# Optimization experiments

Hardware: AMD Instinct MI355X
Metric: run time of the kernel (lower is better)

Reference implementation:

```python
import jax, jax.numpy as jnp
import numpy as np

B, P, G, E = 8, 32, 128, 32
S, SUB = 1024, 768
HD = E // 2              # gene head dim = 16
LAMBDA_INIT = 0.8 - 0.6 * float(np.exp(-0.3 * 0))  # depth=0 -> 0.2
SCALING = HD ** -0.5


def stable_softmax(x, axis=-1, eps=1e-8):
    x_max = jnp.max(x, axis=axis, keepdims=True)
    x_exp = jnp.exp(x - x_max)
    return x_exp / (jnp.sum(x_exp, axis=axis, keepdims=True) + eps)


def setup_inputs() -> dict:
    key = jax.random.key(0)
    ks = jax.random.split(key, 12)
    std_q = (1.0 / E) ** 0.5
    std_k = (1.0 / SUB) ** 0.5
    return {
        "query": jax.random.normal(ks[0], (B, P, G, E), jnp.float32),
        "key": jax.random.normal(ks[1], (B, S, SUB), jnp.float32),
        "query_mask": jax.random.randint(ks[2], (B, P, G), 0, 2).astype(bool),
        "key_mask": jax.random.randint(ks[3], (B, S), 0, 2).astype(bool),
        "Wq": jax.random.normal(ks[4], (E, E), jnp.float32) * std_q,
        "Wk": jax.random.normal(ks[5], (SUB, E), jnp.float32) * std_k,
        "Wv": jax.random.normal(ks[6], (SUB, E), jnp.float32) * std_k,
        "Wo": jax.random.normal(ks[7], (E, E), jnp.float32) * std_q,
        "lq1": jax.random.normal(ks[8], (HD,), jnp.float32) * 0.1,
        "lk1": jax.random.normal(ks[9], (HD,), jnp.float32) * 0.1,
        "lq2": jax.random.normal(ks[10], (HD,), jnp.float32) * 0.1,
        "lk2": jax.random.normal(ks[11], (HD,), jnp.float32) * 0.1,
        "rms_w": jnp.ones((E,), jnp.float32),
    }


def reference(query, key, query_mask, key_mask, Wq, Wk, Wv, Wo,
              lq1, lk1, lq2, lk2, rms_w):
    b, p, g, e = query.shape
    L = p * g
    s = key.shape[1]

    gene_flat = query.reshape(b, L, e)
    Q = (gene_flat @ Wq).reshape(b, L, 2, HD).transpose(0, 2, 1, 3)  # [B,2,L,hd]
    K = (key @ Wk).reshape(b, s, 2, HD).transpose(0, 2, 1, 3)        # [B,2,S,hd]
    V = key @ Wv                                                     # [B,S,2*hd]

    scores = jnp.einsum("bhld,bhsd->bhls", Q * SCALING, K)           # [B,2,L,S]

    qm = query_mask.reshape(b, L)                                    # [B,L]
    combined = qm[:, None, :, None] & key_mask[:, None, None, :]     # [B,1,L,S]
    scores = jnp.where(combined, scores, -1e20)

    attn = stable_softmax(scores, axis=-1)                           # [B,2,L,S]

    lam1 = jnp.exp(jnp.sum(lq1 * lk1))
    lam2 = jnp.exp(jnp.sum(lq2 * lk2))
    lam_full = lam1 - lam2 + LAMBDA_INIT

    diff = attn[:, 0] - lam_full * attn[:, 1]                        # [B,L,S]
    diff = diff - jnp.min(diff, axis=-1, keepdims=True) + 1e-5
    diff = jnp.where(qm[:, :, None], diff, 0.0)
    diff = jnp.where(key_mask[:, None, :], diff, 0.0)

    attn_out = jnp.einsum("bls,bse->ble", diff, V)                   # [B,L,E]

    # RMSNorm over last dim (2*hd = E), eps=1e-5, elementwise affine
    rms = jax.lax.rsqrt(jnp.mean(attn_out * attn_out, axis=-1, keepdims=True) + 1e-5)
    attn_out = attn_out * rms * rms_w
    attn_out = attn_out * (1.0 - LAMBDA_INIT)

    out = (attn_out @ Wo).reshape(b, p, g, e)
    return out, diff.reshape(b, p, g, s)
```

## Files before the change

### kernel.cpp

```cpp
#include <hip/hip_runtime.h>

namespace {

typedef __attribute__((ext_vector_type(8))) short short8v;
typedef __attribute__((ext_vector_type(4))) float f32x4;
typedef __attribute__((ext_vector_type(4))) unsigned int uint4v;

constexpr int kB = 8;
constexpr int kS = 1024;
constexpr int kSUB = 768;
constexpr int kL = 4096;
constexpr float kQScale = 0.25f * 1.44269504088896340736f;
constexpr float kLamInit = 0.2f;
constexpr float kOutScale = 0.8f;
constexpr float kShift = 64.f;

__device__ __forceinline__ unsigned short f2bf(float x) {
  unsigned u = __float_as_uint(x);
  return (unsigned short)((u + 0x7FFFu + ((u >> 16) & 1u)) >> 16);
}

__device__ __forceinline__ float fast_exp2(float x) {
#if __has_builtin(__builtin_amdgcn_exp2f)
  return __builtin_amdgcn_exp2f(x);
#else
  return exp2f(x);
#endif
}

__device__ __forceinline__ int load_mask(const void* p, long i, int fmt) {
  if (fmt == 1) return (int)((const unsigned char*)p)[i];
  if (fmt == 2) return (int)(((const int*)p)[2 * i] != 0);
  return ((const int*)p)[i];
}

__global__ __launch_bounds__(256) void prep_kernel(
    const float* __restrict__ Wk, const float* __restrict__ Wv,
    const unsigned char* __restrict__ qm, unsigned short* __restrict__ WkT,
    unsigned short* __restrict__ WvT, int* __restrict__ flag) {
  if (blockIdx.x < 192) {
    int idx = blockIdx.x * 256 + threadIdx.x;
    if (idx < 24576) {
      const int k = idx >> 5, c = idx & 31;
      WkT[c * 768 + k] = f2bf(Wk[idx]);
    } else {
      idx -= 24576;
      const int k = idx >> 5, c = idx & 31;
      WvT[c * 768 + k] = f2bf(Wv[idx]);
    }
  } else {
    __shared__ int any14, any47;
    if (threadIdx.x == 0) { any14 = 0; any47 = 0; }
    __syncthreads();
    int l14 = 0, l47 = 0;
    for (int i = threadIdx.x; i < 16384; i += 256) {
      const unsigned char v = qm[i];
      if (v && (i & 3)) l14 = 1;
      if (v && ((i & 7) >= 4)) l47 = 1;
    }
    if (l14) atomicOr(&any14, 1);
    if (l47) atomicOr(&any47, 1);
    __syncthreads();
    if (threadIdx.x == 0) *flag = any14 ? 1 : (any47 ? 0 : 2);
  }
}

__global__ __launch_bounds__(256) void proj_kv_kernel(
    const float* __restrict__ key, const unsigned short* __restrict__ WkT,
    const unsigned short* __restrict__ WvT, unsigned short* __restrict__ Kbf,
    unsigned short* __restrict__ Vt) {
  __shared__ float comb[2][64][20];
  const int t = threadIdx.x;
  const int wv = t >> 6, lane = t & 63;
  const int r15 = lane & 15, g = lane >> 4;
  const int grp = wv >> 1;
  const int half = wv & 1;
  const int row = blockIdx.x * 32 + grp * 16 + r15;
  const int kbase = half * 384;
  const float* kp = &key[(size_t)row * kSUB + kbase];
  const f32x4 zf = {0.f, 0.f, 0.f, 0.f};
  f32x4 aK0 = zf, aK1 = zf, aV0 = zf, aV1 = zf;
#pragma unroll 4
  for (int ks = 0; ks < 384; ks += 32) {
    const f32x4 lo = *(const f32x4*)&kp[ks + g * 8];
    const f32x4 hi = *(const f32x4*)&kp[ks + g * 8 + 4];
    short8v a;
#pragma unroll
    for (int j = 0; j < 4; ++j) {
      a[j] = (short)f2bf(lo[j]);
      a[4 + j] = (short)f2bf(hi[j]);
    }
    const int ko = kbase + ks + g * 8;
    const short8v bk0 = *(const short8v*)&WkT[(size_t)r15 * 768 + ko];
    const short8v bk1 = *(const short8v*)&WkT[(size_t)(16 + r15) * 768 + ko];
    const short8v bv0 = *(const short8v*)&WvT[(size_t)r15 * 768 + ko];
    const short8v bv1 = *(const short8v*)&WvT[(size_t)(16 + r15) * 768 + ko];
    aK0 = __builtin_amdgcn_mfma_f32_16x16x32_bf16(a, bk0, aK0, 0, 0, 0);
    aK1 = __builtin_amdgcn_mfma_f32_16x16x32_bf16(a, bk1, aK1, 0, 0, 0);
    aV0 = __builtin_amdgcn_mfma_f32_16x16x32_bf16(a, bv0, aV0, 0, 0, 0);
    aV1 = __builtin_amdgcn_mfma_f32_16x16x32_bf16(a, bv1, aV1, 0, 0, 0);
  }
  if (half == 1) {
    *(f32x4*)&comb[grp][lane][0] = aK0;
    *(f32x4*)&comb[grp][lane][4] = aK1;
    *(f32x4*)&comb[grp][lane][8] = aV0;
    *(f32x4*)&comb[grp][lane][12] = aV1;
  }
  __syncthreads();
  if (half == 0) {
    aK0 += *(const f32x4*)&comb[grp][lane][0];
    aK1 += *(const f32x4*)&comb[grp][lane][4];
    aV0 += *(const f32x4*)&comb[grp][lane][8];
    aV1 += *(const f32x4*)&comb[grp][lane][12];
    const int orow = blockIdx.x * 32 + grp * 16 + g * 4;
#pragma unroll
    for (int jj = 0; jj < 4; ++jj) {
      const int r = orow + jj;
      Kbf[(size_t)r * 32 + r15] = f2bf(aK0[jj]);
      Kbf[(size_t)r * 32 + 16 + r15] = f2bf(aK1[jj]);
      const int bb = r >> 10, s = r & 1023;
      Vt[((size_t)bb * 32 + r15) * kS + s] = f2bf(aV0[jj]);
      Vt[((size_t)bb * 32 + 16 + r15) * kS + s] = f2bf(aV1[jj]);
    }
  }
}

__global__ __launch_bounds__(512, 2) void attn_kernel(
    const float* __restrict__ query, const float* __restrict__ Wq,
    const unsigned short* __restrict__ Kbf,
    const unsigned short* __restrict__ Vt, const void* __restrict__ qmask,
    const void* __restrict__ kmask, const float* __restrict__ lq1,
    const float* __restrict__ lk1, const float* __restrict__ lq2,
    const float* __restrict__ lk2, const float* __restrict__ rmsw,
    const float* __restrict__ Wo, const int* __restrict__ mflag,
    float* __restrict__ out, float* __restrict__ diff) {
  extern __shared__ __align__(16) unsigned short kfl[];

  __shared__ __align__(16) float ubuf[5120];
  __shared__ __align__(16) unsigned short qlds[128][40];
  __shared__ unsigned kmp_lds[256];
  __shared__ float sWo[32][32];
  __shared__ float srw[32];
  __shared__ int qmS[128];
  __shared__ float slam;

  float* const sWq = ubuf;
  float* const sQi = ubuf + 1024;
  float* const nxlds = ubuf;

  const int t = threadIdx.x;
  const int lane = t & 63;
  const int w = t >> 6;
  const int r15 = lane & 15;
  const int g = lane >> 4;
  const int b = blockIdx.x >> 5;
  const int rowbase = b * kL + (blockIdx.x & 31) * 128;
  const int kvb = b * kS;
  const int fmt = *mflag;

  if (t < 256) {
    *(f32x4*)(sWq + 4 * t) = *(const f32x4*)(Wq + 4 * t);
    *(f32x4*)(&sWo[0][0] + 4 * t) = *(const f32x4*)(Wo + 4 * t);
    const long base = (long)kvb + 4 * t;
    const unsigned m0 = load_mask(kmask, base + 0, fmt) ? 1u : 0u;
    const unsigned m1 = load_mask(kmask, base + 1, fmt) ? 1u : 0u;
    const unsigned m2 = load_mask(kmask, base + 2, fmt) ? 1u : 0u;
    const unsigned m3 = load_mask(kmask, base + 3, fmt) ? 1u : 0u;
    kmp_lds[t] = m0 | (m1 << 8) | (m2 << 16) | (m3 << 24);
  }
  *(f32x4*)(sQi + 8 * t) = *(const f32x4*)(query + (size_t)rowbase * 32 + 8 * t);
  *(f32x4*)(sQi + 8 * t + 4) =
      *(const f32x4*)(query + (size_t)rowbase * 32 + 8 * t + 4);
#pragma unroll
  for (int p = 0; p < 8; ++p) {
    const int i = t + 512 * p;
    const int row = i >> 2, qtr = i & 3;
    *(short8v*)&kfl[row * 40 + qtr * 8] =
        *(const short8v*)&Kbf[((size_t)(kvb + row)) * 32 + qtr * 8];
  }
  if (t < 128) qmS[t] = load_mask(qmask, (long)rowbase + t, fmt);
  if (t < 32) srw[t] = rmsw[t];
  if (t == 0) {
    float a = 0.f, c2 = 0.f;
#pragma unroll
    for (int i = 0; i < 16; ++i) {
      a += lq1[i] * lk1[i];
      c2 += lq2[i] * lk2[i];
    }
    slam = expf(a) - expf(c2) + kLamInit;
  }
  __syncthreads();

#pragma unroll
  for (int p = 0; p < 8; ++p) {
    const int idx = t + 512 * p;
    const int row = idx >> 5, col = idx & 31;
    float a = 0.f;
#pragma unroll
    for (int k = 0; k < 32; ++k) a += sQi[row * 32 + k] * sWq[k * 32 + col];
    qlds[row][col] = f2bf(a * kQScale);
  }
  __syncthreads();

  const short8v z8 = {0, 0, 0, 0, 0, 0, 0, 0};
  const f32x4 zf = {0.f, 0.f, 0.f, 0.f};
  const float lam = slam;
  const int qm = qmS[w * 16 + r15];
  const int wrow = rowbase + w * 16;

  short8v qa0 = z8, qa1 = z8;
  if (lane < 32) {
    qa0 = *(const short8v*)&qlds[w * 16 + r15][g * 8];
    qa1 = *(const short8v*)&qlds[w * 16 + r15][16 + g * 8];
  }

  f32x4 s0v = zf, s1v = zf;
  for (int sl = 0; sl < 8; ++sl) {
#pragma unroll
    for (int c = 0; c < 8; ++c) {
      const int srow = sl * 128 + c * 16 + r15;
      short8v kb0 = z8, kb1 = z8;
      if (lane < 32) {
        kb0 = *(const short8v*)&kfl[srow * 40 + g * 8];
        kb1 = *(const short8v*)&kfl[srow * 40 + 16 + g * 8];
      }
      const f32x4 a0 =
          __builtin_amdgcn_mfma_f32_16x16x32_bf16(kb0, qa0, zf, 0, 0, 0);
      const f32x4 a1 =
          __builtin_amdgcn_mfma_f32_16x16x32_bf16(kb1, qa1, zf, 0, 0, 0);
      const unsigned km = kmp_lds[sl * 32 + c * 4 + g];
#pragma unroll
      for (int jj = 0; jj < 4; ++jj) {
        const int mbit = (km >> (8 * jj)) & 1u;
        s0v[jj] += mbit ? fast_exp2(a0[jj] - kShift) : 0.f;
        s1v[jj] += mbit ? fast_exp2(a1[jj] - kShift) : 0.f;
      }
    }
  }
  float s0 = (s0v[0] + s0v[1]) + (s0v[2] + s0v[3]);
  float s1 = (s1v[0] + s1v[1]) + (s1v[2] + s1v[3]);
  s0 += __shfl_xor(s0, 16);
  s0 += __shfl_xor(s0, 32);
  s1 += __shfl_xor(s1, 16);
  s1 += __shfl_xor(s1, 32);
  const float f0 = 1.f / (s0 + 1e-37f);
  const float nf1 = -lam / (s1 + 1e-37f);

  f32x4 dmn = {3.0e38f, 3.0e38f, 3.0e38f, 3.0e38f};
  for (int sl = 0; sl < 8; ++sl) {
#pragma unroll
    for (int c = 0; c < 8; ++c) {
      const int srow = sl * 128 + c * 16 + r15;
      short8v kb0 = z8, kb1 = z8;
      if (lane < 32) {
        kb0 = *(const short8v*)&kfl[srow * 40 + g * 8];
        kb1 = *(const short8v*)&kfl[srow * 40 + 16 + g * 8];
      }
      const f32x4 a0 =
          __builtin_amdgcn_mfma_f32_16x16x32_bf16(kb0, qa0, zf, 0, 0, 0);
      const f32x4 a1 =
          __builtin_amdgcn_mfma_f32_16x16x32_bf16(kb1, qa1, zf, 0, 0, 0);
      const unsigned km = kmp_lds[sl * 32 + c * 4 + g];
#pragma unroll
      for (int jj = 0; jj < 4; ++jj) {
        const int mbit = (km >> (8 * jj)) & 1u;
        const float e0 = mbit ? fast_exp2(a0[jj] - kShift) : 0.f;
        const float e1 = mbit ? fast_exp2(a1[jj] - kShift) : 0.f;
        dmn[jj] = fminf(dmn[jj], fmaf(e0, f0, nf1 * e1));
      }
    }
  }
  float dm = fminf(fminf(dmn[0], dmn[1]), fminf(dmn[2], dmn[3]));
  dm = fminf(dm, __shfl_xor(dm, 16));
  dm = fminf(dm, __shfl_xor(dm, 32));
  const float rmin = dm;

  f32x4 pv0 = zf, pv1 = zf;
  const int sl0 = ((g & 1) << 5) + r15;
  const int sl1 = sl0 + 16;
  const bool hi = (g >> 1) != 0;
  for (int sl = 0; sl < 8; ++sl) {
    short8v vt0[4], vt1[4];
#pragma unroll
    for (int kc = 0; kc < 4; ++kc) {
      const int soff = sl * 128 + kc * 32 + g * 8;
      vt0[kc] = *(const short8v*)&Vt[((size_t)(b * 32 + r15)) * kS + soff];
      vt1[kc] = *(const short8v*)&Vt[((size_t)(b * 32 + 16 + r15)) * kS + soff];
    }
    unsigned pkx[8], pky[8];
#pragma unroll
    for (int c = 0; c < 8; ++c) {
      const int srow = sl * 128 + c * 16 + r15;
      short8v kb0 = z8, kb1 = z8;
      if (lane < 32) {
        kb0 = *(const short8v*)&kfl[srow * 40 + g * 8];
        kb1 = *(const short8v*)&kfl[srow * 40 + 16 + g * 8];
      }
      const f32x4 a0 =
          __builtin_amdgcn_mfma_f32_16x16x32_bf16(kb0, qa0, zf, 0, 0, 0);
      const f32x4 a1 =
          __builtin_amdgcn_mfma_f32_16x16x32_bf16(kb1, qa1, zf, 0, 0, 0);
      const unsigned km = kmp_lds[sl * 32 + c * 4 + g];
      f32x4 fd;
#pragma unroll
      for (int jj = 0; jj < 4; ++jj) {
        const int mbit = (km >> (8 * jj)) & 1u;
        const float e0 = mbit ? fast_exp2(a0[jj] - kShift) : 0.f;
        const float e1 = mbit ? fast_exp2(a1[jj] - kShift) : 0.f;
        const float d = fmaf(e0, f0, nf1 * e1);
        fd[jj] = (qm && mbit) ? d - rmin + 1e-5f : 0.f;
      }
      pkx[c] = (unsigned)f2bf(fd[0]) | ((unsigned)f2bf(fd[1]) << 16);
      pky[c] = (unsigned)f2bf(fd[2]) | ((unsigned)f2bf(fd[3]) << 16);
      *(f32x4*)&diff[((size_t)(wrow + r15)) * kS + sl * 128 + c * 16 + g * 4] =
          fd;
    }
#pragma unroll
    for (int kc = 0; kc < 4; ++kc) {
      const unsigned x0a = (unsigned)__shfl((int)pkx[2 * kc], sl0);
      const unsigned y0a = (unsigned)__shfl((int)pky[2 * kc], sl0);
      const unsigned x0b = (unsigned)__shfl((int)pkx[2 * kc], sl1);
      const unsigned y0b = (unsigned)__shfl((int)pky[2 * kc], sl1);
      const unsigned x1a = (unsigned)__shfl((int)pkx[2 * kc + 1], sl0);
      const unsigned y1a = (unsigned)__shfl((int)pky[2 * kc + 1], sl0);
      const unsigned x1b = (unsigned)__shfl((int)pkx[2 * kc + 1], sl1);
      const unsigned y1b = (unsigned)__shfl((int)pky[2 * kc + 1], sl1);
      uint4v avw;
      avw.x = hi ? x1a : x0a;
      avw.y = hi ? y1a : y0a;
      avw.z = hi ? x1b : x0b;
      avw.w = hi ? y1b : y0b;
      const short8v av = *(const short8v*)&avw;
      pv0 = __builtin_amdgcn_mfma_f32_16x16x32_bf16(av, vt0[kc], pv0, 0, 0, 0);
      pv1 = __builtin_amdgcn_mfma_f32_16x16x32_bf16(av, vt1[kc], pv1, 0, 0, 0);
    }
  }

  float* const nxw = nxlds + w * (16 * 36);
#pragma unroll
  for (int jj = 0; jj < 4; ++jj) {
    float ss = pv0[jj] * pv0[jj] + pv1[jj] * pv1[jj];
    ss += __shfl_xor(ss, 1);
    ss += __shfl_xor(ss, 2);
    ss += __shfl_xor(ss, 4);
    ss += __shfl_xor(ss, 8);
    const float rms = 1.0f / sqrtf(ss * (1.f / 32.f) + 1e-5f);
    nxw[(g * 4 + jj) * 36 + r15] = pv0[jj] * rms * srw[r15] * kOutScale;
    nxw[(g * 4 + jj) * 36 + 16 + r15] =
        pv1[jj] * rms * srw[16 + r15] * kOutScale;
  }
  asm volatile("s_waitcnt lgkmcnt(0)" ::: "memory");

  {
    const int q2 = lane >> 2;
    const int cg = (lane & 3) * 8;
    float o[8] = {0.f, 0.f, 0.f, 0.f, 0.f, 0.f, 0.f, 0.f};
#pragma unroll
    for (int e = 0; e < 32; ++e) {
      const float nv = nxw[q2 * 36 + e];
#pragma unroll
      for (int j = 0; j < 8; ++j) o[j] += nv * sWo[e][cg + j];
    }
    f32x4 olo = {o[0], o[1], o[2], o[3]};
    f32x4 ohi = {o[4], o[5], o[6], o[7]};
    *(f32x4*)&out[((size_t)(wrow + q2)) * 32 + cg] = olo;
    *(f32x4*)&out[((size_t)(wrow + q2)) * 32 + cg + 4] = ohi;
  }
}

}

extern "C" void kernel_launch(void* const* d_in, const int* in_sizes, int n_in,
                              void* d_out, int out_size, void* d_ws,
                              size_t ws_size, hipStream_t stream) {
  const float* query = (const float*)d_in[0];
  const float* key = (const float*)d_in[1];
  const void* qmask = d_in[2];
  const void* kmask = d_in[3];
  const float* Wq = (const float*)d_in[4];
  const float* Wk = (const float*)d_in[5];
  const float* Wv = (const float*)d_in[6];
  const float* Wo = (const float*)d_in[7];
  const float* lq1 = (const float*)d_in[8];
  const float* lk1 = (const float*)d_in[9];
  const float* lq2 = (const float*)d_in[10];
  const float* lk2 = (const float*)d_in[11];
  const float* rmsw = (const float*)d_in[12];

  unsigned short* Kbf = (unsigned short*)d_ws;
  unsigned short* Vt = Kbf + (size_t)kB * kS * 32;
  unsigned short* WkT = Vt + (size_t)kB * kS * 32;
  unsigned short* WvT = WkT + (size_t)32 * 768;
  int* mflag = (int*)(WvT + (size_t)32 * 768);

  float* outp = (float*)d_out;
  float* diffp = outp + (size_t)kB * kL * 32;

  prep_kernel<<<dim3(193), dim3(256), 0, stream>>>(
      Wk, Wv, (const unsigned char*)qmask, WkT, WvT, mflag);
  proj_kv_kernel<<<dim3(kB * kS / 32), dim3(256), 0, stream>>>(key, WkT, WvT,
                                                               Kbf, Vt);
  attn_kernel<<<dim3(kB * (kL / 128)), dim3(512), 81920, stream>>>(
      query, Wq, Kbf, Vt, qmask, kmask, lq1, lk1, lq2, lk2, rmsw, Wo, mflag,
      outp, diffp);
}
```

Before: 104.1 us.

## Split key dimension across wave pairs and read K directly from global

The attention kernel now handles 32 query rows per 256-thread block instead of 128 rows per 512-thread block. Each pair of waves splits the 1024 keys in half, and the halves are combined through LDS reductions for the softmax sums, the row minimum and the PV accumulators. The 80 KB dynamic LDS staging of K is removed, and K is loaded from global/L2 on each pass. This cuts LDS use so more blocks can be resident and gives four times as many blocks, at the cost of repeated global K reads, extra block barriers, and half the waves sitting idle during the output projection.

```diff
diff --git a/kernel.cpp b/kernel.cpp
--- a/kernel.cpp
+++ b/kernel.cpp
@@ -125,7 +125,7 @@
   }
 }
 
-__global__ __launch_bounds__(512, 2) void attn_kernel(
+__global__ __launch_bounds__(256, 4) void attn_kernel(
     const float* __restrict__ query, const float* __restrict__ Wq,
     const unsigned short* __restrict__ Kbf,
     const unsigned short* __restrict__ Vt, const void* __restrict__ qmask,
@@ -134,14 +134,15 @@
     const float* __restrict__ lk2, const float* __restrict__ rmsw,
     const float* __restrict__ Wo, const int* __restrict__ mflag,
     float* __restrict__ out, float* __restrict__ diff) {
-  extern __shared__ __align__(16) unsigned short kfl[];
-
-  __shared__ __align__(16) float ubuf[5120];
-  __shared__ __align__(16) unsigned short qlds[128][40];
+  __shared__ __align__(16) float ubuf[2048];
+  __shared__ __align__(16) unsigned short qlds[32][40];
   __shared__ unsigned kmp_lds[256];
   __shared__ float sWo[32][32];
+  __shared__ float redA[4][2][16];
+  __shared__ float redB[4][16];
+  __shared__ float pvred[4][16][33];
   __shared__ float srw[32];
-  __shared__ int qmS[128];
+  __shared__ int qmS[32];
   __shared__ float slam;
 
   float* const sWq = ubuf;
@@ -151,14 +152,16 @@
   const int t = threadIdx.x;
   const int lane = t & 63;
   const int w = t >> 6;
+  const int group = w >> 1;
+  const int shalf = w & 1;
   const int r15 = lane & 15;
   const int g = lane >> 4;
-  const int b = blockIdx.x >> 5;
-  const int rowbase = b * kL + (blockIdx.x & 31) * 128;
+  const int b = blockIdx.x >> 7;
+  const int rowbase = b * kL + (blockIdx.x & 127) * 32;
   const int kvb = b * kS;
   const int fmt = *mflag;
 
-  if (t < 256) {
+  {
     *(f32x4*)(sWq + 4 * t) = *(const f32x4*)(Wq + 4 * t);
     *(f32x4*)(&sWo[0][0] + 4 * t) = *(const f32x4*)(Wo + 4 * t);
     const long base = (long)kvb + 4 * t;
@@ -167,19 +170,13 @@
     const unsigned m2 = load_mask(kmask, base + 2, fmt) ? 1u : 0u;
     const unsigned m3 = load_mask(kmask, base + 3, fmt) ? 1u : 0u;
     kmp_lds[t] = m0 | (m1 << 8) | (m2 << 16) | (m3 << 24);
-  }
-  *(f32x4*)(sQi + 8 * t) = *(const f32x4*)(query + (size_t)rowbase * 32 + 8 * t);
-  *(f32x4*)(sQi + 8 * t + 4) =
-      *(const f32x4*)(query + (size_t)rowbase * 32 + 8 * t + 4);
-#pragma unroll
-  for (int p = 0; p < 8; ++p) {
-    const int i = t + 512 * p;
-    const int row = i >> 2, qtr = i & 3;
-    *(short8v*)&kfl[row * 40 + qtr * 8] =
-        *(const short8v*)&Kbf[((size_t)(kvb + row)) * 32 + qtr * 8];
-  }
-  if (t < 128) qmS[t] = load_mask(qmask, (long)rowbase + t, fmt);
-  if (t < 32) srw[t] = rmsw[t];
+    *(f32x4*)(sQi + 4 * t) =
+        *(const f32x4*)(query + (size_t)rowbase * 32 + 4 * t);
+  }
+  if (t < 32) {
+    qmS[t] = load_mask(qmask, (long)rowbase + t, fmt);
+    srw[t] = rmsw[t];
+  }
   if (t == 0) {
     float a = 0.f, c2 = 0.f;
 #pragma unroll
@@ -192,8 +189,8 @@
   __syncthreads();
 
 #pragma unroll
-  for (int p = 0; p < 8; ++p) {
-    const int idx = t + 512 * p;
+  for (int p = 0; p < 4; ++p) {
+    const int idx = t + 256 * p;
     const int row = idx >> 5, col = idx & 31;
     float a = 0.f;
 #pragma unroll
@@ -205,30 +202,33 @@
   const short8v z8 = {0, 0, 0, 0, 0, 0, 0, 0};
   const f32x4 zf = {0.f, 0.f, 0.f, 0.f};
   const float lam = slam;
-  const int qm = qmS[w * 16 + r15];
-  const int wrow = rowbase + w * 16;
+  const int qm = qmS[group * 16 + r15];
+  const int wrow = rowbase + group * 16;
+  const int sbase = shalf * 512;
 
   short8v qa0 = z8, qa1 = z8;
   if (lane < 32) {
-    qa0 = *(const short8v*)&qlds[w * 16 + r15][g * 8];
-    qa1 = *(const short8v*)&qlds[w * 16 + r15][16 + g * 8];
+    qa0 = *(const short8v*)&qlds[group * 16 + r15][g * 8];
+    qa1 = *(const short8v*)&qlds[group * 16 + r15][16 + g * 8];
   }
 
   f32x4 s0v = zf, s1v = zf;
-  for (int sl = 0; sl < 8; ++sl) {
+#pragma unroll
+  for (int sl = 0; sl < 4; ++sl) {
 #pragma unroll
     for (int c = 0; c < 8; ++c) {
-      const int srow = sl * 128 + c * 16 + r15;
+      const int srow = sbase + sl * 128 + c * 16 + r15;
       short8v kb0 = z8, kb1 = z8;
       if (lane < 32) {
-        kb0 = *(const short8v*)&kfl[srow * 40 + g * 8];
-        kb1 = *(const short8v*)&kfl[srow * 40 + 16 + g * 8];
+        const unsigned short* kr = &Kbf[((size_t)(kvb + srow)) * 32];
+        kb0 = *(const short8v*)&kr[g * 8];
+        kb1 = *(const short8v*)&kr[16 + g * 8];
       }
       const f32x4 a0 =
           __builtin_amdgcn_mfma_f32_16x16x32_bf16(kb0, qa0, zf, 0, 0, 0);
       const f32x4 a1 =
           __builtin_amdgcn_mfma_f32_16x16x32_bf16(kb1, qa1, zf, 0, 0, 0);
-      const unsigned km = kmp_lds[sl * 32 + c * 4 + g];
+      const unsigned km = kmp_lds[shalf * 128 + sl * 32 + c * 4 + g];
 #pragma unroll
       for (int jj = 0; jj < 4; ++jj) {
         const int mbit = (km >> (8 * jj)) & 1u;
@@ -243,24 +243,33 @@
   s0 += __shfl_xor(s0, 32);
   s1 += __shfl_xor(s1, 16);
   s1 += __shfl_xor(s1, 32);
-  const float f0 = 1.f / (s0 + 1e-37f);
-  const float nf1 = -lam / (s1 + 1e-37f);
+  if (lane < 16) {
+    redA[w][0][lane] = s0;
+    redA[w][1][lane] = s1;
+  }
+  __syncthreads();
+  const float s0t = redA[group * 2][0][r15] + redA[group * 2 + 1][0][r15];
+  const float s1t = redA[group * 2][1][r15] + redA[group * 2 + 1][1][r15];
+  const float f0 = 1.f / (s0t + 1e-37f);
+  const float nf1 = -lam / (s1t + 1e-37f);
 
   f32x4 dmn = {3.0e38f, 3.0e38f, 3.0e38f, 3.0e38f};
-  for (int sl = 0; sl < 8; ++sl) {
+#pragma unroll
+  for (int sl = 0; sl < 4; ++sl) {
 #pragma unroll
     for (int c = 0; c < 8; ++c) {
-      const int srow = sl * 128 + c * 16 + r15;
+      const int srow = sbase + sl * 128 + c * 16 + r15;
       short8v kb0 = z8, kb1 = z8;
       if (lane < 32) {
-        kb0 = *(const short8v*)&kfl[srow * 40 + g * 8];
-        kb1 = *(const short8v*)&kfl[srow * 40 + 16 + g * 8];
+        const unsigned short* kr = &Kbf[((size_t)(kvb + srow)) * 32];
+        kb0 = *(const short8v*)&kr[g * 8];
+        kb1 = *(const short8v*)&kr[16 + g * 8];
       }
       const f32x4 a0 =
           __builtin_amdgcn_mfma_f32_16x16x32_bf16(kb0, qa0, zf, 0, 0, 0);
       const f32x4 a1 =
           __builtin_amdgcn_mfma_f32_16x16x32_bf16(kb1, qa1, zf, 0, 0, 0);
-      const unsigned km = kmp_lds[sl * 32 + c * 4 + g];
+      const unsigned km = kmp_lds[shalf * 128 + sl * 32 + c * 4 + g];
 #pragma unroll
       for (int jj = 0; jj < 4; ++jj) {
         const int mbit = (km >> (8 * jj)) & 1u;
@@ -273,34 +282,39 @@
   float dm = fminf(fminf(dmn[0], dmn[1]), fminf(dmn[2], dmn[3]));
   dm = fminf(dm, __shfl_xor(dm, 16));
   dm = fminf(dm, __shfl_xor(dm, 32));
-  const float rmin = dm;
+  if (lane < 16) redB[w][lane] = dm;
+  __syncthreads();
+  const float rmin = fminf(redB[group * 2][r15], redB[group * 2 + 1][r15]);
+  const float rme = rmin - 1e-5f;
 
   f32x4 pv0 = zf, pv1 = zf;
   const int sl0 = ((g & 1) << 5) + r15;
   const int sl1 = sl0 + 16;
   const bool hi = (g >> 1) != 0;
-  for (int sl = 0; sl < 8; ++sl) {
+#pragma unroll
+  for (int sl = 0; sl < 4; ++sl) {
     short8v vt0[4], vt1[4];
 #pragma unroll
     for (int kc = 0; kc < 4; ++kc) {
-      const int soff = sl * 128 + kc * 32 + g * 8;
+      const int soff = sbase + sl * 128 + kc * 32 + g * 8;
       vt0[kc] = *(const short8v*)&Vt[((size_t)(b * 32 + r15)) * kS + soff];
       vt1[kc] = *(const short8v*)&Vt[((size_t)(b * 32 + 16 + r15)) * kS + soff];
     }
     unsigned pkx[8], pky[8];
 #pragma unroll
     for (int c = 0; c < 8; ++c) {
-      const int srow = sl * 128 + c * 16 + r15;
+      const int srow = sbase + sl * 128 + c * 16 + r15;
       short8v kb0 = z8, kb1 = z8;
       if (lane < 32) {
-        kb0 = *(const short8v*)&kfl[srow * 40 + g * 8];
-        kb1 = *(const short8v*)&kfl[srow * 40 + 16 + g * 8];
+        const unsigned short* kr = &Kbf[((size_t)(kvb + srow)) * 32];
+        kb0 = *(const short8v*)&kr[g * 8];
+        kb1 = *(const short8v*)&kr[16 + g * 8];
       }
       const f32x4 a0 =
           __builtin_amdgcn_mfma_f32_16x16x32_bf16(kb0, qa0, zf, 0, 0, 0);
       const f32x4 a1 =
           __builtin_amdgcn_mfma_f32_16x16x32_bf16(kb1, qa1, zf, 0, 0, 0);
-      const unsigned km = kmp_lds[sl * 32 + c * 4 + g];
+      const unsigned km = kmp_lds[shalf * 128 + sl * 32 + c * 4 + g];
       f32x4 fd;
 #pragma unroll
       for (int jj = 0; jj < 4; ++jj) {
@@ -308,12 +322,12 @@
         const float e0 = mbit ? fast_exp2(a0[jj] - kShift) : 0.f;
         const float e1 = mbit ? fast_exp2(a1[jj] - kShift) : 0.f;
         const float d = fmaf(e0, f0, nf1 * e1);
-        fd[jj] = (qm && mbit) ? d - rmin + 1e-5f : 0.f;
-      }
+        fd[jj] = (qm && mbit) ? d - rme : 0.f;
+      }
+      *(f32x4*)&diff[((size_t)(wrow + r15)) * kS + sbase + sl * 128 + c * 16 +
+                     g * 4] = fd;
       pkx[c] = (unsigned)f2bf(fd[0]) | ((unsigned)f2bf(fd[1]) << 16);
       pky[c] = (unsigned)f2bf(fd[2]) | ((unsigned)f2bf(fd[3]) << 16);
-      *(f32x4*)&diff[((size_t)(wrow + r15)) * kS + sl * 128 + c * 16 + g * 4] =
-          fd;
     }
 #pragma unroll
     for (int kc = 0; kc < 4; ++kc) {
@@ -335,23 +349,36 @@
       pv1 = __builtin_amdgcn_mfma_f32_16x16x32_bf16(av, vt1[kc], pv1, 0, 0, 0);
     }
   }
-
-  float* const nxw = nxlds + w * (16 * 36);
 #pragma unroll
   for (int jj = 0; jj < 4; ++jj) {
-    float ss = pv0[jj] * pv0[jj] + pv1[jj] * pv1[jj];
-    ss += __shfl_xor(ss, 1);
-    ss += __shfl_xor(ss, 2);
-    ss += __shfl_xor(ss, 4);
-    ss += __shfl_xor(ss, 8);
-    const float rms = 1.0f / sqrtf(ss * (1.f / 32.f) + 1e-5f);
-    nxw[(g * 4 + jj) * 36 + r15] = pv0[jj] * rms * srw[r15] * kOutScale;
-    nxw[(g * 4 + jj) * 36 + 16 + r15] =
-        pv1[jj] * rms * srw[16 + r15] * kOutScale;
-  }
-  asm volatile("s_waitcnt lgkmcnt(0)" ::: "memory");
-
-  {
+    pvred[w][g * 4 + jj][r15] = pv0[jj];
+    pvred[w][g * 4 + jj][16 + r15] = pv1[jj];
+  }
+  __syncthreads();
+
+  if (shalf == 0) {
+    f32x4 pv0c, pv1c;
+#pragma unroll
+    for (int jj = 0; jj < 4; ++jj) {
+      pv0c[jj] = pvred[w][g * 4 + jj][r15] + pvred[w + 1][g * 4 + jj][r15];
+      pv1c[jj] =
+          pvred[w][g * 4 + jj][16 + r15] + pvred[w + 1][g * 4 + jj][16 + r15];
+    }
+    float* const nxw = nxlds + group * (16 * 36);
+#pragma unroll
+    for (int jj = 0; jj < 4; ++jj) {
+      float ss = pv0c[jj] * pv0c[jj] + pv1c[jj] * pv1c[jj];
+      ss += __shfl_xor(ss, 1);
+      ss += __shfl_xor(ss, 2);
+      ss += __shfl_xor(ss, 4);
+      ss += __shfl_xor(ss, 8);
+      const float rms = 1.0f / sqrtf(ss * (1.f / 32.f) + 1e-5f);
+      nxw[(g * 4 + jj) * 36 + r15] = pv0c[jj] * rms * srw[r15] * kOutScale;
+      nxw[(g * 4 + jj) * 36 + 16 + r15] =
+          pv1c[jj] * rms * srw[16 + r15] * kOutScale;
+    }
+    asm volatile("s_waitcnt lgkmcnt(0)" ::: "memory");
+
     const int q2 = lane >> 2;
     const int cg = (lane & 3) * 8;
     float o[8] = {0.f, 0.f, 0.f, 0.f, 0.f, 0.f, 0.f, 0.f};
@@ -400,7 +427,7 @@
       Wk, Wv, (const unsigned char*)qmask, WkT, WvT, mflag);
   proj_kv_kernel<<<dim3(kB * kS / 32), dim3(256), 0, stream>>>(key, WkT, WvT,
                                                                Kbf, Vt);
-  attn_kernel<<<dim3(kB * (kL / 128)), dim3(512), 81920, stream>>>(
+  attn_kernel<<<dim3(kB * (kL / 32)), dim3(256), 0, stream>>>(
       query, Wq, Kbf, Vt, qmask, kmask, lq1, lk1, lq2, lk2, rmsw, Wo, mflag,
       outp, diffp);
 }
```

Result: slower. 392.2 us (+276.8%).
